# Optimization experiments

Hardware: AMD Instinct MI355X
Metric: run time of the kernel (lower is better)

The kernel has to match this reference:

```python
import jax, jax.numpy as jnp
import numpy as np

TEMPERATURE = 0.1
USE_RANKS = True
USE_SCORES = True
RANK_WEIGHT = 0.1
SCORE_WEIGHT = 0.01
NUM_GROUPS = 1024  # question_ids in [0, NUM_GROUPS)
BATCH = 4096
DIM = 1024


def setup_inputs() -> dict:
    key = jax.random.key(0)
    k1, k2, k3, k4, k5 = jax.random.split(key, 5)
    q_embeddings = jax.random.normal(k1, (BATCH, DIM), dtype=jnp.float32)
    a_embeddings = jax.random.normal(k2, (BATCH, DIM), dtype=jnp.float32)
    question_ids = jax.random.randint(k3, (BATCH,), 0, NUM_GROUPS, dtype=jnp.int32)
    ranks = jax.random.uniform(k4, (BATCH,), dtype=jnp.float32) * 8.0  # ordinal-ish ranks
    scores = jax.random.uniform(k5, (BATCH,), dtype=jnp.float32)
    return {
        "q_embeddings": q_embeddings,
        "a_embeddings": a_embeddings,
        "question_ids": question_ids,
        "ranks": ranks,
        "scores": scores,
    }


def _positive_weights(question_ids, ranks, scores):
    """Per-sample positive weight, normalized to sum to 1 within each question group."""
    w = jnp.ones_like(ranks)
    if USE_RANKS:
        w = w * jnp.exp(-RANK_WEIGHT * ranks)
    if USE_SCORES:
        gmax = jax.ops.segment_max(scores, question_ids, num_segments=NUM_GROUPS)
        gmin = jax.ops.segment_min(scores, question_ids, num_segments=NUM_GROUPS)
        denom = gmax[question_ids] - gmin[question_ids]
        norm = jnp.where(denom > 0, (scores - gmin[question_ids]) / jnp.where(denom > 0, denom, 1.0), 0.0)
        w = w * jnp.exp(SCORE_WEIGHT * norm)
    wsum = jax.ops.segment_sum(w, question_ids, num_segments=NUM_GROUPS)[question_ids]
    gsize = jax.ops.segment_sum(jnp.ones_like(w), question_ids, num_segments=NUM_GROUPS)[question_ids]
    w = jnp.where(wsum > 0, w / jnp.where(wsum > 0, wsum, 1.0), 1.0 / gsize)
    return w


def reference(q_embeddings, a_embeddings, question_ids, ranks, scores):
    B = q_embeddings.shape[0]
    # [B, B] similarity, one fused batched log-softmax over rows
    similarity = jnp.matmul(q_embeddings, a_embeddings.T) / TEMPERATURE
    log_probs = jax.nn.log_softmax(similarity, axis=1)
    # same-group mask: sample j is a positive for row i iff same question id
    same = (question_ids[:, None] == question_ids[None, :])
    w = _positive_weights(question_ids, ranks, scores)  # [B], group-normalized
    # loss_i = -sum_{j in group(i)} w_j * log_probs[i, j]; total averaged over batch
    per_row = -jnp.sum(jnp.where(same, w[None, :] * log_probs, 0.0), axis=1)
    loss = jnp.sum(per_row) / B
    # accuracy: argmax of each row lands inside the row's group
    pred = jnp.argmax(similarity, axis=1)
    acc = jnp.mean((question_ids[pred] == question_ids).astype(jnp.float32))
    return loss, acc
```

## Files before the change

kernel.cpp:

```cpp
#include <hip/hip_runtime.h>
#include <hip/hip_bf16.h>
#include <math.h>

#define BATCH   4096
#define DIM     1024
#define NGROUPS 1024
#define INV_T   10.0f
#define RANK_W  0.1f
#define SCORE_W 0.01f

#define BI 128
#define BJ 256
#define KC 32
#define NFRAG_Q (BI/16)
#define NFRAG   (BI/16 + BJ/16)
#define FRAG_ELEMS 512

typedef float  floatx4 __attribute__((ext_vector_type(4)));
typedef __bf16 bf16x8  __attribute__((ext_vector_type(8)));
typedef __bf16 bf16x4  __attribute__((ext_vector_type(4)));

#define ASYNC_COPY16(gptr, lptr)                                              \
    __builtin_amdgcn_global_load_lds(                                         \
        (const __attribute__((address_space(1))) void*)(gptr),                \
        (__attribute__((address_space(3))) void*)(lptr), 16, 0, 0)

__global__ __launch_bounds__(256) void prep_kernel(
    const float* __restrict__ Q, const float* __restrict__ A,
    __bf16* __restrict__ Qb, __bf16* __restrict__ Ab,
    const int* __restrict__ qid, const float* __restrict__ ranks,
    const float* __restrict__ scores, float* __restrict__ w)
{
    const int tid = threadIdx.x;

    if (blockIdx.x >= NGROUPS) {
        const int cid = blockIdx.x - NGROUPS;
        const int n4  = BATCH * DIM / 4;
        for (int i = cid * 256 + tid; i < n4; i += 1024 * 256) {
            float4 v = ((const float4*)Q)[i];
            bf16x4 b;
            b[0] = (__bf16)v.x; b[1] = (__bf16)v.y;
            b[2] = (__bf16)v.z; b[3] = (__bf16)v.w;
            ((bf16x4*)Qb)[i] = b;
            v = ((const float4*)A)[i];
            b[0] = (__bf16)v.x; b[1] = (__bf16)v.y;
            b[2] = (__bf16)v.z; b[3] = (__bf16)v.w;
            ((bf16x4*)Ab)[i] = b;
        }
        return;
    }

    const int g = blockIdx.x, lane = tid & 63, wv = tid >> 6;
    __shared__ float rmax[4], rmin[4], rsum[4];

    float gmax = -INFINITY, gmin = INFINITY;
    for (int j = tid; j < BATCH; j += 256) {
        if (qid[j] == g) {
            float s = scores[j];
            gmax = fmaxf(gmax, s);
            gmin = fminf(gmin, s);
        }
    }
    #pragma unroll
    for (int d = 1; d < 64; d <<= 1) {
        gmax = fmaxf(gmax, __shfl_xor(gmax, d, 64));
        gmin = fminf(gmin, __shfl_xor(gmin, d, 64));
    }
    if (lane == 0) { rmax[wv] = gmax; rmin[wv] = gmin; }
    __syncthreads();
    gmax = fmaxf(fmaxf(rmax[0], rmax[1]), fmaxf(rmax[2], rmax[3]));
    gmin = fminf(fminf(rmin[0], rmin[1]), fminf(rmin[2], rmin[3]));
    const float denom     = gmax - gmin;
    const float inv_denom = (denom > 0.f) ? 1.f / denom : 0.f;

    float lsum = 0.f;
    for (int j = tid; j < BATCH; j += 256) {
        if (qid[j] == g) {
            float norm = (scores[j] - gmin) * inv_denom;
            float u = __expf(-RANK_W * ranks[j] + SCORE_W * norm);
            w[j] = u;
            lsum += u;
        }
    }
    #pragma unroll
    for (int d = 1; d < 64; d <<= 1) lsum += __shfl_xor(lsum, d, 64);
    if (lane == 0) rsum[wv] = lsum;
    __syncthreads();
    const float wsum = rsum[0] + rsum[1] + rsum[2] + rsum[3];
    const float inv  = (wsum > 0.f) ? 1.f / wsum : 0.f;
    for (int j = tid; j < BATCH; j += 256) {
        if (qid[j] == g) w[j] *= inv;
    }
}

__global__ __launch_bounds__(512, 4) void fused_simloss_kernel(
    const __bf16* __restrict__ Qb, const __bf16* __restrict__ Ab,
    const int* __restrict__ qid, const float* __restrict__ w,
    float* __restrict__ Pm, float* __restrict__ Pl, float* __restrict__ Ps,
    float* __restrict__ Pbv, int* __restrict__ Pbi)
{
    __shared__ __bf16 sbuf[2][NFRAG * FRAG_ELEMS];

    const int jb = blockIdx.x, ib = blockIdx.y;
    const int i0 = ib * BI, j0 = jb * BJ;
    const int tid = threadIdx.x, wid = tid >> 6, lane = tid & 63;
    const int wm = wid >> 2, wn = wid & 3;
    const int quad = lane >> 4, l16 = lane & 15;

    floatx4 acc[4][4];
    #pragma unroll
    for (int m = 0; m < 4; ++m)
        #pragma unroll
        for (int n = 0; n < 4; ++n)
            #pragma unroll
            for (int c = 0; c < 4; ++c) acc[m][n][c] = 0.f;

    const int lr = lane & 15;
    const int lk = (lane >> 4) * 8;
    const __bf16* src[3];
    #pragma unroll
    for (int c = 0; c < 3; ++c) {
        const int f = wid * 3 + c;
        src[c] = (f < NFRAG_Q)
               ? Qb + (size_t)(i0 + f * 16 + lr) * DIM + lk
               : Ab + (size_t)(j0 + (f - NFRAG_Q) * 16 + lr) * DIM + lk;
    }

    #define STAGE(buf, k0)                                                    \
        do {                                                                  \
            _Pragma("unroll")                                                 \
            for (int c = 0; c < 3; ++c)                                       \
                ASYNC_COPY16(src[c] + (k0),                                   \
                             &sbuf[buf][(wid * 3 + c) * FRAG_ELEMS]);         \
        } while (0)

    STAGE(0, 0);

    for (int t = 0; t < DIM / KC; ++t) {
        __syncthreads();
        if (t + 1 < DIM / KC) STAGE((t + 1) & 1, (t + 1) * KC);

        const __bf16* cur = sbuf[t & 1];
        bf16x8 qf[4], af[4];
        #pragma unroll
        for (int mf = 0; mf < 4; ++mf)
            qf[mf] = *(const bf16x8*)&cur[(wm * 4 + mf) * FRAG_ELEMS + lane * 8];
        #pragma unroll
        for (int nf = 0; nf < 4; ++nf)
            af[nf] = *(const bf16x8*)&cur[(NFRAG_Q + wn * 4 + nf) * FRAG_ELEMS + lane * 8];
        #pragma unroll
        for (int nf = 0; nf < 4; ++nf)
            #pragma unroll
            for (int mf = 0; mf < 4; ++mf)
                acc[mf][nf] = __builtin_amdgcn_mfma_f32_16x16x32_bf16(
                    qf[mf], af[nf], acc[mf][nf], 0, 0, 0);
    }
    #undef STAGE

    int cq[4]; float cw[4];
    #pragma unroll
    for (int n = 0; n < 4; ++n) {
        int col = j0 + wn * 64 + n * 16 + l16;
        cq[n] = qid[col];
        cw[n] = w[col];
    }
    const int slice = jb * 4 + wn;

    #pragma unroll
    for (int m = 0; m < 4; ++m) {
        #pragma unroll
        for (int reg = 0; reg < 4; ++reg) {
            const int row = i0 + wm * 64 + m * 16 + quad * 4 + reg;
            const int rq  = qid[row];

            float v[4];
            #pragma unroll
            for (int n = 0; n < 4; ++n) v[n] = acc[m][n][reg] * INV_T;

            float lm = fmaxf(fmaxf(v[0], v[1]), fmaxf(v[2], v[3]));
            float ll = __expf(v[0] - lm) + __expf(v[1] - lm) +
                       __expf(v[2] - lm) + __expf(v[3] - lm);
            float ls = 0.f;
            #pragma unroll
            for (int n = 0; n < 4; ++n) ls += (cq[n] == rq) ? cw[n] * v[n] : 0.f;

            float bv = v[0];
            int   bi = j0 + wn * 64 + l16;
            #pragma unroll
            for (int n = 1; n < 4; ++n) {
                int c = j0 + wn * 64 + n * 16 + l16;
                if (v[n] > bv) { bv = v[n]; bi = c; }
            }

            #pragma unroll
            for (int d = 1; d < 16; d <<= 1) {
                float om  = __shfl_xor(lm, d, 64);
                float ol  = __shfl_xor(ll, d, 64);
                float os  = __shfl_xor(ls, d, 64);
                float obv = __shfl_xor(bv, d, 64);
                int   obi = __shfl_xor(bi, d, 64);
                float nm = fmaxf(lm, om);
                ll = ll * __expf(lm - nm) + ol * __expf(om - nm);
                lm = nm;
                ls += os;
                if (obv > bv || (obv == bv && obi < bi)) { bv = obv; bi = obi; }
            }
            if (l16 == 0) {
                int idx = row * 64 + slice;
                Pm[idx] = lm; Pl[idx] = ll; Ps[idx] = ls;
                Pbv[idx] = bv; Pbi[idx] = bi;
            }
        }
    }
}

__global__ __launch_bounds__(256) void row_reduce_kernel(
    const float* __restrict__ Pm, const float* __restrict__ Pl,
    const float* __restrict__ Ps, const float* __restrict__ Pbv,
    const int* __restrict__ Pbi, const int* __restrict__ qid,
    float* __restrict__ per_row, float* __restrict__ ind)
{
    const int r    = blockIdx.x * 4 + (threadIdx.x >> 6);
    const int lane = threadIdx.x & 63;
    const int idx  = r * 64 + lane;

    float m = Pm[idx], l = Pl[idx], s = Ps[idx], bv = Pbv[idx];
    int   bi = Pbi[idx];

    #pragma unroll
    for (int d = 1; d < 64; d <<= 1) {
        float om  = __shfl_xor(m, d, 64);
        float ol  = __shfl_xor(l, d, 64);
        float os  = __shfl_xor(s, d, 64);
        float obv = __shfl_xor(bv, d, 64);
        int   obi = __shfl_xor(bi, d, 64);
        float nm = fmaxf(m, om);
        l = l * __expf(m - nm) + ol * __expf(om - nm);
        m = nm;
        s += os;
        if (obv > bv || (obv == bv && obi < bi)) { bv = obv; bi = obi; }
    }
    if (lane == 0) {
        per_row[r] = (m + logf(l)) - s;
        ind[r]     = (qid[bi] == qid[r]) ? 1.f : 0.f;
    }
}

__global__ __launch_bounds__(1024) void final_kernel(
    const float* __restrict__ per_row, const float* __restrict__ ind,
    float* __restrict__ out)
{
    const int tid = threadIdx.x;
    float s1 = 0.f, s2 = 0.f;
    for (int i = tid; i < BATCH; i += 1024) { s1 += per_row[i]; s2 += ind[i]; }
    #pragma unroll
    for (int d = 1; d < 64; d <<= 1) {
        s1 += __shfl_xor(s1, d, 64);
        s2 += __shfl_xor(s2, d, 64);
    }
    __shared__ float r1[16], r2[16];
    if ((tid & 63) == 0) { r1[tid >> 6] = s1; r2[tid >> 6] = s2; }
    __syncthreads();
    if (tid == 0) {
        float t1 = 0.f, t2 = 0.f;
        #pragma unroll
        for (int i = 0; i < 16; ++i) { t1 += r1[i]; t2 += r2[i]; }
        out[0] = t1 / (float)BATCH;
        out[1] = t2 / (float)BATCH;
    }
}

extern "C" void kernel_launch(void* const* d_in, const int* in_sizes, int n_in,
                              void* d_out, int out_size, void* d_ws, size_t ws_size,
                              hipStream_t stream)
{
    const float* Q      = (const float*)d_in[0];
    const float* A      = (const float*)d_in[1];
    const int*   qid    = (const int*)d_in[2];
    const float* ranks  = (const float*)d_in[3];
    const float* scores = (const float*)d_in[4];
    float* out = (float*)d_out;

    __bf16* Qb = (__bf16*)d_ws;
    __bf16* Ab = Qb + (size_t)BATCH * DIM;
    float* w       = (float*)(Ab + (size_t)BATCH * DIM);
    float* Pm      = w + BATCH;
    float* Pl      = Pm + BATCH * 64;
    float* Ps      = Pl + BATCH * 64;
    float* Pbv     = Ps + BATCH * 64;
    int*   Pbi     = (int*)(Pbv + BATCH * 64);
    float* per_row = (float*)(Pbi + BATCH * 64);
    float* ind     = per_row + BATCH;

    prep_kernel<<<2048, 256, 0, stream>>>(Q, A, Qb, Ab, qid, ranks, scores, w);

    dim3 grid(BATCH / BJ, BATCH / BI);
    fused_simloss_kernel<<<grid, 512, 0, stream>>>(Qb, Ab, qid, w, Pm, Pl, Ps, Pbv, Pbi);

    row_reduce_kernel<<<BATCH / 4, 256, 0, stream>>>(Pm, Pl, Ps, Pbv, Pbi, qid, per_row, ind);

    final_kernel<<<1, 1024, 0, stream>>>(per_row, ind, out);
}
```

Baseline: 162.5 us.

## Enlarge similarity tile to 256x256, remap blocks per XCD, fold final reduction into atomics

Doubles the row tile of the fused bf16 MFMA similarity kernel to 256x256 with 1024-thread blocks. Each wave now stages two fragments instead of three, so more of each loaded Q/A panel is reused. Block indices are remapped so blocks sharing an XCD work on nearby row and column panels, to improve L2 locality. The separate final reduction kernel is removed: row_reduce accumulates directly into the output with atomics after a memset. The costs are a grid of only 256 blocks (about one per CU), possible register pressure under the new launch bounds, and nondeterministic float atomic ordering.

```diff
diff --git a/kernel.cpp b/kernel.cpp
--- a/kernel.cpp
+++ b/kernel.cpp
@@ -9,7 +9,7 @@
 #define RANK_W  0.1f
 #define SCORE_W 0.01f
 
-#define BI 128
+#define BI 256
 #define BJ 256
 #define KC 32
 #define NFRAG_Q (BI/16)
@@ -93,7 +93,7 @@
     }
 }
 
-__global__ __launch_bounds__(512, 4) void fused_simloss_kernel(
+__global__ __launch_bounds__(1024, 4) void fused_simloss_kernel(
     const __bf16* __restrict__ Qb, const __bf16* __restrict__ Ab,
     const int* __restrict__ qid, const float* __restrict__ w,
     float* __restrict__ Pm, float* __restrict__ Pl, float* __restrict__ Ps,
@@ -101,8 +101,12 @@
 {
     __shared__ __bf16 sbuf[2][NFRAG * FRAG_ELEMS];
 
-    const int jb = blockIdx.x, ib = blockIdx.y;
+    const int bid = blockIdx.x;
+    const int xcd = bid & 7, s = bid >> 3;
+    const int ib = (xcd >> 1) * 4 + (s & 3);
+    const int jb = (xcd & 1) * 8 + (s >> 2);
     const int i0 = ib * BI, j0 = jb * BJ;
+
     const int tid = threadIdx.x, wid = tid >> 6, lane = tid & 63;
     const int wm = wid >> 2, wn = wid & 3;
     const int quad = lane >> 4, l16 = lane & 15;
@@ -117,10 +121,10 @@
 
     const int lr = lane & 15;
     const int lk = (lane >> 4) * 8;
-    const __bf16* src[3];
-    #pragma unroll
-    for (int c = 0; c < 3; ++c) {
-        const int f = wid * 3 + c;
+    const __bf16* src[2];
+    #pragma unroll
+    for (int c = 0; c < 2; ++c) {
+        const int f = wid * 2 + c;
         src[c] = (f < NFRAG_Q)
                ? Qb + (size_t)(i0 + f * 16 + lr) * DIM + lk
                : Ab + (size_t)(j0 + (f - NFRAG_Q) * 16 + lr) * DIM + lk;
@@ -129,9 +133,9 @@
     #define STAGE(buf, k0)                                                    \
         do {                                                                  \
             _Pragma("unroll")                                                 \
-            for (int c = 0; c < 3; ++c)                                       \
+            for (int c = 0; c < 2; ++c)                                       \
                 ASYNC_COPY16(src[c] + (k0),                                   \
-                             &sbuf[buf][(wid * 3 + c) * FRAG_ELEMS]);         \
+                             &sbuf[buf][(wid * 2 + c) * FRAG_ELEMS]);         \
         } while (0)
 
     STAGE(0, 0);
@@ -218,9 +222,10 @@
     const float* __restrict__ Pm, const float* __restrict__ Pl,
     const float* __restrict__ Ps, const float* __restrict__ Pbv,
     const int* __restrict__ Pbi, const int* __restrict__ qid,
-    float* __restrict__ per_row, float* __restrict__ ind)
-{
-    const int r    = blockIdx.x * 4 + (threadIdx.x >> 6);
+    float* __restrict__ out)
+{
+    const int wv   = threadIdx.x >> 6;
+    const int r    = blockIdx.x * 4 + wv;
     const int lane = threadIdx.x & 63;
     const int idx  = r * 64 + lane;
 
@@ -240,33 +245,18 @@
         s += os;
         if (obv > bv || (obv == bv && obi < bi)) { bv = obv; bi = obi; }
     }
+
+    __shared__ float sm[4], si[4];
     if (lane == 0) {
-        per_row[r] = (m + logf(l)) - s;
-        ind[r]     = (qid[bi] == qid[r]) ? 1.f : 0.f;
-    }
-}
-
-__global__ __launch_bounds__(1024) void final_kernel(
-    const float* __restrict__ per_row, const float* __restrict__ ind,
-    float* __restrict__ out)
-{
-    const int tid = threadIdx.x;
-    float s1 = 0.f, s2 = 0.f;
-    for (int i = tid; i < BATCH; i += 1024) { s1 += per_row[i]; s2 += ind[i]; }
-    #pragma unroll
-    for (int d = 1; d < 64; d <<= 1) {
-        s1 += __shfl_xor(s1, d, 64);
-        s2 += __shfl_xor(s2, d, 64);
-    }
-    __shared__ float r1[16], r2[16];
-    if ((tid & 63) == 0) { r1[tid >> 6] = s1; r2[tid >> 6] = s2; }
+        sm[wv] = (m + logf(l)) - s;
+        si[wv] = (qid[bi] == qid[r]) ? 1.f : 0.f;
+    }
     __syncthreads();
-    if (tid == 0) {
-        float t1 = 0.f, t2 = 0.f;
-        #pragma unroll
-        for (int i = 0; i < 16; ++i) { t1 += r1[i]; t2 += r2[i]; }
-        out[0] = t1 / (float)BATCH;
-        out[1] = t2 / (float)BATCH;
+    if (threadIdx.x == 0) {
+        float t1 = (sm[0] + sm[1]) + (sm[2] + sm[3]);
+        float t2 = (si[0] + si[1]) + (si[2] + si[3]);
+        atomicAdd(&out[0], t1 * (1.f / (float)BATCH));
+        atomicAdd(&out[1], t2 * (1.f / (float)BATCH));
     }
 }
 
@@ -289,15 +279,12 @@
     float* Ps      = Pl + BATCH * 64;
     float* Pbv     = Ps + BATCH * 64;
     int*   Pbi     = (int*)(Pbv + BATCH * 64);
-    float* per_row = (float*)(Pbi + BATCH * 64);
-    float* ind     = per_row + BATCH;
+
+    hipMemsetAsync(out, 0, 2 * sizeof(float), stream);
 
     prep_kernel<<<2048, 256, 0, stream>>>(Q, A, Qb, Ab, qid, ranks, scores, w);
 
-    dim3 grid(BATCH / BJ, BATCH / BI);
-    fused_simloss_kernel<<<grid, 512, 0, stream>>>(Qb, Ab, qid, w, Pm, Pl, Ps, Pbv, Pbi);
-
-    row_reduce_kernel<<<BATCH / 4, 256, 0, stream>>>(Pm, Pl, Ps, Pbv, Pbi, qid, per_row, ind);
-
-    final_kernel<<<1, 1024, 0, stream>>>(per_row, ind, out);
-}
+    fused_simloss_kernel<<<256, 1024, 0, stream>>>(Qb, Ab, qid, w, Pm, Pl, Ps, Pbv, Pbi);
+
+    row_reduce_kernel<<<BATCH / 4, 256, 0, stream>>>(Pm, Pl, Ps, Pbv, Pbi, qid, out);
+}
```

After: 177.5 us. 9.2% more time.
